# Kernel tuning notes

Hardware: AMD Instinct MI355X
Metric: run time of the kernel (lower is better)

Reference implementation:

```python
import jax, jax.numpy as jnp
import numpy as np

D_MODEL = 1024
N_HEADS = 16
D_K = D_MODEL // N_HEADS


def setup_inputs() -> dict:
    key = jax.random.key(0)
    k1, k2, k3 = jax.random.split(key, 3)
    x = jax.random.normal(k1, (4, 2048, D_MODEL), dtype=jnp.float32)
    # torch nn.Linear(d, 3d, bias=False): y = x @ W.T ; we store W.T directly as (in, out)
    w_qkv = jax.random.normal(k2, (D_MODEL, 3 * D_MODEL), dtype=jnp.float32) * (1.0 / np.sqrt(D_MODEL))
    w_out = jax.random.normal(k3, (D_MODEL, D_MODEL), dtype=jnp.float32) * (1.0 / np.sqrt(D_MODEL))
    return {"x": x, "w_qkv": w_qkv, "w_out": w_out}


def reference(x, w_qkv, w_out):
    B, T, D = x.shape
    qkv = jnp.einsum('btd,de->bte', x, w_qkv)  # (B,T,3D)
    q, k, v = jnp.split(qkv, 3, axis=-1)
    # split heads -> (B,H,T,d_k)
    def split_heads(t):
        return t.reshape(B, T, N_HEADS, D_K).transpose(0, 2, 1, 3)
    q, k, v = split_heads(q), split_heads(k), split_heads(v)
    scale = 1.0 / np.sqrt(D_K).astype(np.float32)
    scores = jnp.einsum('bhqd,bhkd->bhqk', q, k) * scale  # (B,H,T,T)
    causal = jnp.triu(jnp.full((T, T), -jnp.inf, dtype=scores.dtype), k=1)
    scores = scores + causal[None, None]
    weights = jax.nn.softmax(scores, axis=-1)
    attn = jnp.einsum('bhqk,bhkd->bhqd', weights, v)
    attn = attn.transpose(0, 2, 1, 3).reshape(B, T, D)
    return jnp.einsum('btd,de->bte', attn, w_out)
```

## Files before the change

### kernel.cpp

```cpp
#include <hip/hip_runtime.h>
#include <hip/hip_bf16.h>

typedef short short8 __attribute__((ext_vector_type(8)));
typedef float f32x4 __attribute__((ext_vector_type(4)));
typedef float f32x16 __attribute__((ext_vector_type(16)));

#define MFMA16(a, b, c) __builtin_amdgcn_mfma_f32_16x16x32_bf16((a), (b), (c), 0, 0, 0)
#define MFMA32(a, b, c) __builtin_amdgcn_mfma_f32_32x32x16_bf16((a), (b), (c), 0, 0, 0)

#define GLOAD16(gp, lp)                                                    \
    __builtin_amdgcn_global_load_lds(                                      \
        (const __attribute__((address_space(1))) unsigned int*)(gp),       \
        (__attribute__((address_space(3))) unsigned int*)(lp), 16, 0, 0)

__device__ __forceinline__ unsigned short f2b(float x) {
    unsigned int u = __float_as_uint(x);
    unsigned int r = u + 0x7FFFu + ((u >> 16) & 1u);
    return (unsigned short)(r >> 16);
}

#if __has_builtin(__builtin_amdgcn_cvt_pk_bf16_f32)
__device__ __forceinline__ unsigned pack2(float a, float b) {
    auto v = __builtin_amdgcn_cvt_pk_bf16_f32(a, b);
    unsigned u;
    __builtin_memcpy(&u, &v, 4);
    return u;
}
#else
__device__ __forceinline__ unsigned pack2(float a, float b) {
    return (unsigned)f2b(a) | ((unsigned)f2b(b) << 16);
}
#endif

__global__ __launch_bounds__(256) void cast4_kernel(const float* __restrict__ in,
                                                    unsigned short* __restrict__ out,
                                                    int n4) {
    int i = blockIdx.x * 256 + threadIdx.x;
    if (i < n4) {
        float4 v = ((const float4*)in)[i];
        ushort4 o;
        o.x = f2b(v.x); o.y = f2b(v.y); o.z = f2b(v.z); o.w = f2b(v.w);
        ((ushort4*)out)[i] = o;
    }
}

__global__ __launch_bounds__(256) void transpose_cast_f32(const float* __restrict__ in,
                                                          unsigned short* __restrict__ out,
                                                          int K, int N) {
    __shared__ unsigned short Ls[64 * 66];
    const int k0 = blockIdx.y * 64, n0 = blockIdx.x * 64;
    const int tid = threadIdx.x;
    const int krow = tid >> 4, nc4 = (tid & 15) * 4;
#pragma unroll
    for (int p = 0; p < 4; p++) {
        float4 v = *(const float4*)(in + (size_t)(k0 + krow + p * 16) * N + n0 + nc4);
        unsigned* d32 = (unsigned*)(Ls + (krow + p * 16) * 66 + nc4);
        d32[0] = pack2(v.x, v.y);
        d32[1] = pack2(v.z, v.w);
    }
    __syncthreads();
    const int n = tid >> 3, kc = (tid & 7) * 8;
#pragma unroll
    for (int p = 0; p < 2; p++) {
        int nn = n + p * 32;
        unsigned short w[8];
#pragma unroll
        for (int j = 0; j < 8; j++) w[j] = Ls[(kc + j) * 66 + nn];
        *(short8*)(out + (size_t)(n0 + nn) * K + k0 + kc) = *(short8*)w;
    }
}

__global__ __launch_bounds__(512, 2) void gemm_qkv(const unsigned short* __restrict__ A,
                                                   const unsigned short* __restrict__ Bt,
                                                   unsigned short* __restrict__ Qb,
                                                   unsigned short* __restrict__ Kb,
                                                   unsigned short* __restrict__ Vt) {
    __shared__ __align__(16) unsigned short smem[65536];

    const int tid  = threadIdx.x;
    const int wave = tid >> 6;
    const int lane = tid & 63;
    const int l32  = lane & 31;
    const int hi   = lane >> 5;
    const int wr   = wave >> 2;
    const int wc   = wave & 3;

    const int bid = blockIdx.x;
    const int sid = (bid & 7) * 48 + (bid >> 3);
    const int bx  = sid % 12;
    const int by  = sid / 12;
    const int m0 = by * 256;
    const int n0 = bx * 256;

    const int srow = tid >> 3;
    const int cswz = (((tid & 7) ^ ((tid >> 3) & 7)) * 8);
    const unsigned short* gA = A  + (size_t)(m0 + srow) * 1024 + cswz;
    const unsigned short* gB = Bt + (size_t)(n0 + srow) * 1024 + cswz;

#define STAGE_A(buf, h, kt) do {                                              \
        const unsigned short* _g = gA + (size_t)((h) * 128) * 1024 + (kt) * 64; \
        unsigned short* _l = smem + (buf) * 16384 + (h) * 8192 + wave * 512;  \
        GLOAD16(_g, _l);                                                      \
        GLOAD16(_g + 65536, _l + 4096);                                       \
    } while (0)
#define STAGE_B(buf, h, kt) do {                                              \
        const unsigned short* _g = gB + (size_t)((h) * 128) * 1024 + (kt) * 64; \
        unsigned short* _l = smem + 32768 + (buf) * 16384 + (h) * 8192 + wave * 512; \
        GLOAD16(_g, _l);                                                      \
        GLOAD16(_g + 65536, _l + 4096);                                       \
    } while (0)

    const int sw7  = l32 & 7;
    const int aoff = (wr * 128 + l32) * 64;
    const int boff = (wc * 64 + l32) * 64;

    f32x16 acc[4][2] = {};

    STAGE_A(0, 0, 0); STAGE_A(0, 1, 0); STAGE_B(0, 0, 0); STAGE_B(0, 1, 0);
    STAGE_B(1, 0, 1); STAGE_B(1, 1, 1); STAGE_A(1, 0, 1);
    asm volatile("s_waitcnt vmcnt(6)" ::: "memory");
    __builtin_amdgcn_s_barrier();

#pragma unroll
    for (int t = 0; t < 16; ++t) {
        const int b = t & 1;
        const unsigned short* Ab = smem + b * 16384;
        const unsigned short* Bb = smem + 32768 + b * 16384;

        short8 afLo[2][4], afHi[2][4], bf0[4], bf1[4];

#pragma unroll
        for (int rf = 0; rf < 2; ++rf)
#pragma unroll
            for (int ks = 0; ks < 4; ++ks)
                afLo[rf][ks] = *(const short8*)(Ab + aoff + rf * 2048 + (((ks * 2 + hi) ^ sw7) * 8));
#pragma unroll
        for (int ks = 0; ks < 4; ++ks)
            bf0[ks] = *(const short8*)(Bb + boff + (((ks * 2 + hi) ^ sw7) * 8));
        if (t + 1 < 16) STAGE_A(b ^ 1, 1, t + 1);
        __builtin_amdgcn_s_barrier();
        asm volatile("s_waitcnt lgkmcnt(0)" ::: "memory");
        __builtin_amdgcn_s_setprio(1);
#pragma unroll
        for (int ks = 0; ks < 4; ++ks) {
            acc[0][0] = MFMA32(afLo[0][ks], bf0[ks], acc[0][0]);
            acc[1][0] = MFMA32(afLo[1][ks], bf0[ks], acc[1][0]);
        }
        __builtin_amdgcn_s_setprio(0);
        __builtin_amdgcn_s_barrier();

#pragma unroll
        for (int ks = 0; ks < 4; ++ks)
            bf1[ks] = *(const short8*)(Bb + boff + 2048 + (((ks * 2 + hi) ^ sw7) * 8));
        __builtin_amdgcn_s_barrier();
        asm volatile("s_waitcnt lgkmcnt(0)" ::: "memory");
        __builtin_amdgcn_s_setprio(1);
#pragma unroll
        for (int ks = 0; ks < 4; ++ks) {
            acc[0][1] = MFMA32(afLo[0][ks], bf1[ks], acc[0][1]);
            acc[1][1] = MFMA32(afLo[1][ks], bf1[ks], acc[1][1]);
        }
        __builtin_amdgcn_s_setprio(0);
        __builtin_amdgcn_s_barrier();

#pragma unroll
        for (int rf = 0; rf < 2; ++rf)
#pragma unroll
            for (int ks = 0; ks < 4; ++ks)
                afHi[rf][ks] = *(const short8*)(Ab + aoff + (2 + rf) * 2048 + (((ks * 2 + hi) ^ sw7) * 8));
        if (t + 2 < 16) { STAGE_B(b, 0, t + 2); STAGE_B(b, 1, t + 2); }
        __builtin_amdgcn_s_barrier();
        asm volatile("s_waitcnt lgkmcnt(0)" ::: "memory");
        __builtin_amdgcn_s_setprio(1);
#pragma unroll
        for (int ks = 0; ks < 4; ++ks) {
            acc[2][0] = MFMA32(afHi[0][ks], bf0[ks], acc[2][0]);
            acc[3][0] = MFMA32(afHi[1][ks], bf0[ks], acc[3][0]);
        }
        __builtin_amdgcn_s_setprio(0);
        __builtin_amdgcn_s_barrier();

        if (t + 2 < 16) {
            STAGE_A(b, 0, t + 2);
            asm volatile("s_waitcnt vmcnt(6)" ::: "memory");
        } else {
            asm volatile("s_waitcnt vmcnt(0)" ::: "memory");
        }
        __builtin_amdgcn_s_barrier();
        __builtin_amdgcn_s_setprio(1);
#pragma unroll
        for (int ks = 0; ks < 4; ++ks) {
            acc[2][1] = MFMA32(afHi[0][ks], bf1[ks], acc[2][1]);
            acc[3][1] = MFMA32(afHi[1][ks], bf1[ks], acc[3][1]);
        }
        __builtin_amdgcn_s_setprio(0);
        __builtin_amdgcn_s_barrier();
    }
#undef STAGE_A
#undef STAGE_B

    if (n0 < 2048) {
        unsigned short* outp = (n0 < 1024) ? Qb : Kb;
        const int cb = (n0 < 1024) ? n0 : n0 - 1024;
        const float QS = (n0 < 1024) ? 0.125f * 1.44269504f : 1.0f;
#pragma unroll
        for (int rf = 0; rf < 4; ++rf)
#pragma unroll
            for (int cf = 0; cf < 2; ++cf)
#pragma unroll
                for (int r = 0; r < 16; ++r) {
                    int row = m0 + wr * 128 + rf * 32 + (r & 3) + 8 * (r >> 2) + 4 * hi;
                    int col = cb + wc * 64 + cf * 32 + l32;
                    outp[(size_t)row * 1024 + col] = f2b(acc[rf][cf][r] * QS);
                }
    } else {
        const int bb = m0 >> 11, t0b = m0 & 2047;
        const int hbase = (n0 - 2048) >> 6;
        unsigned short* reg = smem + wc * 16384;
#pragma unroll
        for (int rf = 0; rf < 4; ++rf)
#pragma unroll
            for (int cf = 0; cf < 2; ++cf)
#pragma unroll
                for (int rg = 0; rg < 4; ++rg) {
                    const int tl = wr * 128 + rf * 32 + rg * 8 + 4 * hi;
                    const int d  = cf * 32 + l32;
                    const int w  = d * 128 + ((tl >> 1) ^ (4 * (d & 7)));
                    uint2 v;
                    v.x = pack2(acc[rf][cf][4 * rg + 0], acc[rf][cf][4 * rg + 1]);
                    v.y = pack2(acc[rf][cf][4 * rg + 2], acc[rf][cf][4 * rg + 3]);
                    *(uint2*)(reg + 2 * w) = v;
                }
        __syncthreads();
#pragma unroll
        for (int it = 0; it < 16; ++it) {
            const int id = it * 512 + tid;
            const int hh = id >> 11, d = (id >> 5) & 63, k = id & 31;
            const int kb = k >> 2, kl = k & 3;
            const int xx = 4 * (d & 7);
            const unsigned short* bp = smem + hh * 16384 + 2 * (d * 128);
            uint2 lo  = *(const uint2*)(bp + 2 * ((16 * kb + 2 * kl) ^ xx));
            uint2 hi2 = *(const uint2*)(bp + 2 * ((16 * kb + 2 * kl + 8) ^ xx));
            uint2 parts[2] = {lo, hi2};
            short8 v; __builtin_memcpy(&v, parts, 16);
            *(short8*)(Vt + ((size_t)((bb * 16 + hbase + hh) * 64 + d)) * 2048 + t0b + k * 8) = v;
        }
    }
}

__global__ __launch_bounds__(512, 2) void gemm_out(const unsigned short* __restrict__ A,
                                                   const unsigned short* __restrict__ Bt,
                                                   float* __restrict__ C) {
    __shared__ __align__(16) unsigned short smem[49152];

    const int tid  = threadIdx.x;
    const int wave = tid >> 6;
    const int lane = tid & 63;
    const int l32  = lane & 31;
    const int hi   = lane >> 5;
    const int wr   = wave >> 2;
    const int wc   = wave & 3;

    const int bid = blockIdx.x;
    const int sid = (bid & 7) * 32 + (bid >> 3);
    const int bx  = sid & 3;
    const int by  = sid >> 2;
    const int m0 = by * 128;
    const int n0 = bx * 256;

    const int srow = tid >> 3;
    const int cswz = (((tid & 7) ^ ((tid >> 3) & 7)) * 8);
    const unsigned short* gA = A  + (size_t)(m0 + srow) * 1024 + cswz;
    const unsigned short* gB = Bt + (size_t)(n0 + srow) * 1024 + cswz;

#define STAGE_A(buf, h, kt) do {                                              \
        const unsigned short* _g = gA + (size_t)((h) * 64) * 1024 + (kt) * 64; \
        unsigned short* _l = smem + (buf) * 8192 + (h) * 4096 + wave * 512;   \
        GLOAD16(_g, _l);                                                      \
    } while (0)
#define STAGE_B(buf, h, kt) do {                                              \
        const unsigned short* _g = gB + (size_t)((h) * 128) * 1024 + (kt) * 64; \
        unsigned short* _l = smem + 16384 + (buf) * 16384 + (h) * 8192 + wave * 512; \
        GLOAD16(_g, _l);                                                      \
        GLOAD16(_g + 65536, _l + 4096);                                       \
    } while (0)

    const int sw7  = l32 & 7;
    const int aoff = (wr * 64 + l32) * 64;
    const int boff = (wc * 64 + l32) * 64;

    f32x16 acc[2][2] = {};

    STAGE_A(0, 0, 0); STAGE_A(0, 1, 0); STAGE_B(0, 0, 0); STAGE_B(0, 1, 0);
    STAGE_B(1, 0, 1); STAGE_B(1, 1, 1); STAGE_A(1, 0, 1);
    asm volatile("s_waitcnt vmcnt(5)" ::: "memory");
    __builtin_amdgcn_s_barrier();

#pragma unroll
    for (int t = 0; t < 16; ++t) {
        const int b = t & 1;
        const unsigned short* Ab = smem + b * 8192;
        const unsigned short* Bb = smem + 16384 + b * 16384;

        short8 af0[4], af1[4], bf0[4], bf1[4];

#pragma unroll
        for (int ks = 0; ks < 4; ++ks)
            af0[ks] = *(const short8*)(Ab + aoff + (((ks * 2 + hi) ^ sw7) * 8));
#pragma unroll
        for (int ks = 0; ks < 4; ++ks)
            bf0[ks] = *(const short8*)(Bb + boff + (((ks * 2 + hi) ^ sw7) * 8));
        if (t + 1 < 16) STAGE_A(b ^ 1, 1, t + 1);
        __builtin_amdgcn_s_barrier();
        asm volatile("s_waitcnt lgkmcnt(0)" ::: "memory");
        __builtin_amdgcn_s_setprio(1);
#pragma unroll
        for (int ks = 0; ks < 4; ++ks)
            acc[0][0] = MFMA32(af0[ks], bf0[ks], acc[0][0]);
        __builtin_amdgcn_s_setprio(0);
        __builtin_amdgcn_s_barrier();

#pragma unroll
        for (int ks = 0; ks < 4; ++ks)
            bf1[ks] = *(const short8*)(Bb + boff + 2048 + (((ks * 2 + hi) ^ sw7) * 8));
        __builtin_amdgcn_s_barrier();
        asm volatile("s_waitcnt lgkmcnt(0)" ::: "memory");
        __builtin_amdgcn_s_setprio(1);
#pragma unroll
        for (int ks = 0; ks < 4; ++ks)
            acc[0][1] = MFMA32(af0[ks], bf1[ks], acc[0][1]);
        __builtin_amdgcn_s_setprio(0);
        __builtin_amdgcn_s_barrier();

#pragma unroll
        for (int ks = 0; ks < 4; ++ks)
            af1[ks] = *(const short8*)(Ab + aoff + 2048 + (((ks * 2 + hi) ^ sw7) * 8));
        if (t + 2 < 16) { STAGE_B(b, 0, t + 2); STAGE_B(b, 1, t + 2); }
        __builtin_amdgcn_s_barrier();
        asm volatile("s_waitcnt lgkmcnt(0)" ::: "memory");
        __builtin_amdgcn_s_setprio(1);
#pragma unroll
        for (int ks = 0; ks < 4; ++ks)
            acc[1][0] = MFMA32(af1[ks], bf0[ks], acc[1][0]);
        __builtin_amdgcn_s_setprio(0);
        __builtin_amdgcn_s_barrier();

        if (t + 2 < 16) {
            STAGE_A(b, 0, t + 2);
            asm volatile("s_waitcnt vmcnt(5)" ::: "memory");
        } else {
            asm volatile("s_waitcnt vmcnt(0)" ::: "memory");
        }
        __builtin_amdgcn_s_barrier();
        __builtin_amdgcn_s_setprio(1);
#pragma unroll
        for (int ks = 0; ks < 4; ++ks)
            acc[1][1] = MFMA32(af1[ks], bf1[ks], acc[1][1]);
        __builtin_amdgcn_s_setprio(0);
        __builtin_amdgcn_s_barrier();
    }
#undef STAGE_A
#undef STAGE_B

#pragma unroll
    for (int rf = 0; rf < 2; ++rf)
#pragma unroll
        for (int cf = 0; cf < 2; ++cf)
#pragma unroll
            for (int r = 0; r < 16; ++r) {
                int row = m0 + wr * 64 + rf * 32 + (r & 3) + 8 * (r >> 2) + 4 * hi;
                int col = n0 + wc * 64 + cf * 32 + l32;
                C[(size_t)row * 1024 + col] = acc[rf][cf][r];
            }
}

__global__ __launch_bounds__(512, 8) void attention_kernel(const unsigned short* Qb,
                                                           const unsigned short* Kb,
                                                           const unsigned short* Vt,
                                                           unsigned short* attn) {
    const int T = 2048;
    const int bi = blockIdx.x;
    const int qb = 15 - (bi >> 6);
    const int hb = bi & 63;
    const int b = hb >> 4, h = hb & 15;
    const int tid = threadIdx.x, wave = tid >> 6, lane = tid & 63;
    const int l16 = lane & 15, quad = lane >> 4;
    const int qw0 = qb * 128 + wave * 16;

    const unsigned short* Qp  = Qb + (size_t)b * T * 1024 + h * 64;
    const unsigned short* Kp  = Kb + (size_t)b * T * 1024 + h * 64;
    const unsigned short* Vbh = Vt + ((size_t)(b * 16 + h) * 64) * 2048;

    __shared__ __align__(16) unsigned short smem[2][8192];

    short8 qf[2];
#pragma unroll
    for (int kd = 0; kd < 2; kd++)
        qf[kd] = *(const short8*)(Qp + (size_t)(qw0 + l16) * 1024 + kd * 32 + quad * 8);
    asm volatile("" ::: "memory");

    f32x4 o[4] = {};
    f32x4 o_l = {};
    const f32x4 fz = {};

    short8 onesf;
#pragma unroll
    for (int e = 0; e < 8; e++) onesf[e] = (short)0x3F80;

    const int srow = lane >> 2;
    const int scol = (((lane & 3) ^ ((lane >> 3) & 3)) * 8);
    const int sw8  = ((l16 >> 1) & 3) * 8;

    const unsigned short* gs;
    size_t ktstep, jstep;
    int lofs;
    if (wave < 4) {
        const int p = wave >> 1, cp = wave & 1;
        gs = Kp + (size_t)(cp * 32 + srow) * 1024 + p * 32 + scol;
        ktstep = (size_t)64 * 1024; jstep = (size_t)16 * 1024;
        lofs = p * 2048 + cp * 1024;
    } else {
        const int u = wave - 4, th = u >> 1, cp = u & 1;
        gs = Vbh + (size_t)(cp * 32 + srow) * 2048 + th * 32 + scol;
        ktstep = (size_t)64; jstep = (size_t)16 * 2048;
        lofs = 4096 + th * 2048 + cp * 1024;
    }

#define STAGE(bb, kt) do {                                   \
        const unsigned short* _g = gs + (size_t)(kt) * ktstep; \
        unsigned short* _l = &smem[bb][0] + lofs;             \
        GLOAD16(_g, _l);                                      \
        GLOAD16(_g + jstep, _l + 512);                        \
    } while (0)

    STAGE(0, 0);
    const int last = 2 * qb + 1;
    for (int kt = 0; kt <= last; kt++) {
        const int bsel = kt & 1;
        const int tk0 = kt * 64;
        if (kt < last) {
            STAGE(bsel ^ 1, kt + 1);
            asm volatile("s_waitcnt vmcnt(2)" ::: "memory");
        } else {
            asm volatile("s_waitcnt vmcnt(0)" ::: "memory");
        }
        __builtin_amdgcn_s_barrier();
        asm volatile("" ::: "memory");

        const unsigned short* Kb0 = &smem[bsel][0];
        const unsigned short* Kb1 = Kb0 + 2048;
        const unsigned short* Vb0 = Kb0 + 4096;

#pragma unroll
        for (int th = 0; th < 2; th++) {
            const int t0a = tk0 + th * 32;
            if (t0a > qw0 + 15) continue;
            const int t1 = t0a + 16;
            const bool act1 = (t1 <= qw0 + 15);

            f32x4 s0, s1;
            {
                const int row = (th * 2) * 16 + l16;
                short8 kf0 = *(const short8*)(Kb0 + row * 32 + (quad * 8 ^ sw8));
                short8 kf1 = *(const short8*)(Kb1 + row * 32 + (quad * 8 ^ sw8));
                s0 = MFMA16(kf0, qf[0], fz);
                s0 = MFMA16(kf1, qf[1], s0);
            }
            if (act1) {
                const int row = (th * 2 + 1) * 16 + l16;
                short8 kf0 = *(const short8*)(Kb0 + row * 32 + (quad * 8 ^ sw8));
                short8 kf1 = *(const short8*)(Kb1 + row * 32 + (quad * 8 ^ sw8));
                s1 = MFMA16(kf0, qf[0], fz);
                s1 = MFMA16(kf1, qf[1], s1);
            }

            unsigned u00, u01, u10, u11;
            {
                const bool full = (t0a + 15) <= qw0;
                float p[4];
#pragma unroll
                for (int r = 0; r < 4; r++) {
                    float e = __builtin_amdgcn_exp2f(s0[r]);
                    if (!full)
                        e = (t0a + quad * 4 + r <= qw0 + l16) ? e : 0.f;
                    p[r] = e;
                }
                u00 = pack2(p[0], p[1]);
                u01 = pack2(p[2], p[3]);
            }
            if (act1) {
                const bool full = (t1 + 15) <= qw0;
                float p[4];
#pragma unroll
                for (int r = 0; r < 4; r++) {
                    float e = __builtin_amdgcn_exp2f(s1[r]);
                    if (!full)
                        e = (t1 + quad * 4 + r <= qw0 + l16) ? e : 0.f;
                    p[r] = e;
                }
                u10 = pack2(p[0], p[1]);
                u11 = pack2(p[2], p[3]);
            } else {
                u10 = 0; u11 = 0;
            }

            unsigned pb[4] = {u00, u01, u10, u11};
            short8 pf; __builtin_memcpy(&pf, pb, 16);

            __builtin_amdgcn_s_setprio(1);
            o_l = MFMA16(onesf, pf, o_l);
#pragma unroll
            for (int dt = 0; dt < 4; dt++) {
                short8 vf = *(const short8*)(Vb0 + th * 2048 + (dt * 16 + l16) * 32 + (quad * 8 ^ sw8));
                o[dt] = MFMA16(vf, pf, o[dt]);
            }
            __builtin_amdgcn_s_setprio(0);
        }
        asm volatile("" ::: "memory");
        __builtin_amdgcn_s_barrier();
    }
#undef STAGE

    const float rl = 1.f / o_l[0];
    const int q = qw0 + l16;
#pragma unroll
    for (int dt = 0; dt < 4; dt++) {
        ushort4 wv;
        wv.x = f2b(o[dt][0] * rl);
        wv.y = f2b(o[dt][1] * rl);
        wv.z = f2b(o[dt][2] * rl);
        wv.w = f2b(o[dt][3] * rl);
        *(ushort4*)(attn + (size_t)(b * T + q) * 1024 + h * 64 + dt * 16 + quad * 4) = wv;
    }
}

extern "C" void kernel_launch(void* const* d_in, const int* in_sizes, int n_in,
                              void* d_out, int out_size, void* d_ws, size_t ws_size,
                              hipStream_t stream) {
    const float* x     = (const float*)d_in[0];
    const float* w_qkv = (const float*)d_in[1];
    const float* w_out = (const float*)d_in[2];
    float* out = (float*)d_out;

    const int M = 8192, D = 1024, E = 3072;
    const size_t MB = 1048576;

    char* ws = (char*)d_ws;
    unsigned short* xb    = (unsigned short*)ws;
    unsigned short* wqkvT = (unsigned short*)(ws + 16 * MB);
    unsigned short* woutT = (unsigned short*)(ws + 22 * MB);
    unsigned short* Qb    = (unsigned short*)(ws + 24 * MB);
    unsigned short* Kb    = (unsigned short*)(ws + 40 * MB);
    unsigned short* Vt    = (unsigned short*)(ws + 56 * MB);

    cast4_kernel<<<M * D / 4 / 256, 256, 0, stream>>>(x, xb, M * D / 4);
    transpose_cast_f32<<<dim3(E / 64, D / 64), 256, 0, stream>>>(w_qkv, wqkvT, D, E);
    transpose_cast_f32<<<dim3(D / 64, D / 64), 256, 0, stream>>>(w_out, woutT, D, D);

    gemm_qkv<<<dim3(384), 512, 0, stream>>>(xb, wqkvT, Qb, Kb, Vt);

    attention_kernel<<<dim3(1024), 512, 0, stream>>>(Qb, Kb, Vt, Qb);

    gemm_out<<<dim3(256), 512, 0, stream>>>(Qb, woutT, out);
}
```

Before: 248.3 us.

## Split QKV projection into separate QK and V GEMM kernels

Splits the fused QKV GEMM into two launches. gemm_qk handles the Q/K columns with 256 blocks of 256x256 tiles. It swaps the MFMA operands so each lane holds consecutive columns, which allows packed 8-byte bf16 stores instead of scalar 2-byte stores. gemm_v uses 128x256 tiles over 256 blocks for the V columns and keeps the LDS-staged transposed write into Vt. The intent is to balance work against the CU count (384 blocks does not map evenly onto the device) and to speed up the Q/K epilogue, at the cost of an extra kernel launch and reduced reuse in the smaller V tiles.

Result: no change. 245.5 us (-1.2%).

```diff
diff --git a/kernel.cpp b/kernel.cpp
--- a/kernel.cpp
+++ b/kernel.cpp
@@ -70,11 +70,10 @@
     }
 }
 
-__global__ __launch_bounds__(512, 2) void gemm_qkv(const unsigned short* __restrict__ A,
-                                                   const unsigned short* __restrict__ Bt,
-                                                   unsigned short* __restrict__ Qb,
-                                                   unsigned short* __restrict__ Kb,
-                                                   unsigned short* __restrict__ Vt) {
+__global__ __launch_bounds__(512, 2) void gemm_qk(const unsigned short* __restrict__ A,
+                                                  const unsigned short* __restrict__ Bt,
+                                                  unsigned short* __restrict__ Qb,
+                                                  unsigned short* __restrict__ Kb) {
     __shared__ __align__(16) unsigned short smem[65536];
 
     const int tid  = threadIdx.x;
@@ -86,9 +85,9 @@
     const int wc   = wave & 3;
 
     const int bid = blockIdx.x;
-    const int sid = (bid & 7) * 48 + (bid >> 3);
-    const int bx  = sid % 12;
-    const int by  = sid / 12;
+    const int sid = (bid & 7) * 32 + (bid >> 3);
+    const int bx  = sid & 7;
+    const int by  = sid >> 3;
     const int m0 = by * 256;
     const int n0 = bx * 256;
 
@@ -143,8 +142,8 @@
         __builtin_amdgcn_s_setprio(1);
 #pragma unroll
         for (int ks = 0; ks < 4; ++ks) {
-            acc[0][0] = MFMA32(afLo[0][ks], bf0[ks], acc[0][0]);
-            acc[1][0] = MFMA32(afLo[1][ks], bf0[ks], acc[1][0]);
+            acc[0][0] = MFMA32(bf0[ks], afLo[0][ks], acc[0][0]);
+            acc[1][0] = MFMA32(bf0[ks], afLo[1][ks], acc[1][0]);
         }
         __builtin_amdgcn_s_setprio(0);
         __builtin_amdgcn_s_barrier();
@@ -157,8 +156,8 @@
         __builtin_amdgcn_s_setprio(1);
 #pragma unroll
         for (int ks = 0; ks < 4; ++ks) {
-            acc[0][1] = MFMA32(afLo[0][ks], bf1[ks], acc[0][1]);
-            acc[1][1] = MFMA32(afLo[1][ks], bf1[ks], acc[1][1]);
+            acc[0][1] = MFMA32(bf1[ks], afLo[0][ks], acc[0][1]);
+            acc[1][1] = MFMA32(bf1[ks], afLo[1][ks], acc[1][1]);
         }
         __builtin_amdgcn_s_setprio(0);
         __builtin_amdgcn_s_barrier();
@@ -174,8 +173,8 @@
         __builtin_amdgcn_s_setprio(1);
 #pragma unroll
         for (int ks = 0; ks < 4; ++ks) {
-            acc[2][0] = MFMA32(afHi[0][ks], bf0[ks], acc[2][0]);
-            acc[3][0] = MFMA32(afHi[1][ks], bf0[ks], acc[3][0]);
+            acc[2][0] = MFMA32(bf0[ks], afHi[0][ks], acc[2][0]);
+            acc[3][0] = MFMA32(bf0[ks], afHi[1][ks], acc[3][0]);
         }
         __builtin_amdgcn_s_setprio(0);
         __builtin_amdgcn_s_barrier();
@@ -190,8 +189,8 @@
         __builtin_amdgcn_s_setprio(1);
 #pragma unroll
         for (int ks = 0; ks < 4; ++ks) {
-            acc[2][1] = MFMA32(afHi[0][ks], bf1[ks], acc[2][1]);
-            acc[3][1] = MFMA32(afHi[1][ks], bf1[ks], acc[3][1]);
+            acc[2][1] = MFMA32(bf1[ks], afHi[0][ks], acc[2][1]);
+            acc[3][1] = MFMA32(bf1[ks], afHi[1][ks], acc[3][1]);
         }
         __builtin_amdgcn_s_setprio(0);
         __builtin_amdgcn_s_barrier();
@@ -199,52 +198,169 @@
 #undef STAGE_A
 #undef STAGE_B
 
-    if (n0 < 2048) {
-        unsigned short* outp = (n0 < 1024) ? Qb : Kb;
-        const int cb = (n0 < 1024) ? n0 : n0 - 1024;
-        const float QS = (n0 < 1024) ? 0.125f * 1.44269504f : 1.0f;
-#pragma unroll
-        for (int rf = 0; rf < 4; ++rf)
-#pragma unroll
-            for (int cf = 0; cf < 2; ++cf)
-#pragma unroll
-                for (int r = 0; r < 16; ++r) {
-                    int row = m0 + wr * 128 + rf * 32 + (r & 3) + 8 * (r >> 2) + 4 * hi;
-                    int col = cb + wc * 64 + cf * 32 + l32;
-                    outp[(size_t)row * 1024 + col] = f2b(acc[rf][cf][r] * QS);
-                }
-    } else {
-        const int bb = m0 >> 11, t0b = m0 & 2047;
-        const int hbase = (n0 - 2048) >> 6;
-        unsigned short* reg = smem + wc * 16384;
-#pragma unroll
-        for (int rf = 0; rf < 4; ++rf)
-#pragma unroll
-            for (int cf = 0; cf < 2; ++cf)
-#pragma unroll
-                for (int rg = 0; rg < 4; ++rg) {
-                    const int tl = wr * 128 + rf * 32 + rg * 8 + 4 * hi;
-                    const int d  = cf * 32 + l32;
-                    const int w  = d * 128 + ((tl >> 1) ^ (4 * (d & 7)));
-                    uint2 v;
-                    v.x = pack2(acc[rf][cf][4 * rg + 0], acc[rf][cf][4 * rg + 1]);
-                    v.y = pack2(acc[rf][cf][4 * rg + 2], acc[rf][cf][4 * rg + 3]);
-                    *(uint2*)(reg + 2 * w) = v;
-                }
-        __syncthreads();
-#pragma unroll
-        for (int it = 0; it < 16; ++it) {
-            const int id = it * 512 + tid;
-            const int hh = id >> 11, d = (id >> 5) & 63, k = id & 31;
-            const int kb = k >> 2, kl = k & 3;
-            const int xx = 4 * (d & 7);
-            const unsigned short* bp = smem + hh * 16384 + 2 * (d * 128);
-            uint2 lo  = *(const uint2*)(bp + 2 * ((16 * kb + 2 * kl) ^ xx));
-            uint2 hi2 = *(const uint2*)(bp + 2 * ((16 * kb + 2 * kl + 8) ^ xx));
-            uint2 parts[2] = {lo, hi2};
-            short8 v; __builtin_memcpy(&v, parts, 16);
-            *(short8*)(Vt + ((size_t)((bb * 16 + hbase + hh) * 64 + d)) * 2048 + t0b + k * 8) = v;
-        }
+    unsigned short* outp = (n0 < 1024) ? Qb : Kb;
+    const int cb = (n0 < 1024) ? n0 : n0 - 1024;
+    const float QS = (n0 < 1024) ? 0.125f * 1.44269504f : 1.0f;
+#pragma unroll
+    for (int rf = 0; rf < 4; ++rf) {
+        const int row = m0 + wr * 128 + rf * 32 + l32;
+#pragma unroll
+        for (int cf = 0; cf < 2; ++cf)
+#pragma unroll
+            for (int g = 0; g < 4; ++g) {
+                const int col = cb + wc * 64 + cf * 32 + g * 8 + 4 * hi;
+                uint2 v;
+                v.x = pack2(acc[rf][cf][4 * g + 0] * QS, acc[rf][cf][4 * g + 1] * QS);
+                v.y = pack2(acc[rf][cf][4 * g + 2] * QS, acc[rf][cf][4 * g + 3] * QS);
+                *(uint2*)(outp + (size_t)row * 1024 + col) = v;
+            }
+    }
+}
+
+__global__ __launch_bounds__(512, 2) void gemm_v(const unsigned short* __restrict__ A,
+                                                 const unsigned short* __restrict__ Bt,
+                                                 unsigned short* __restrict__ Vt) {
+    __shared__ __align__(16) unsigned short smem[49152];
+
+    const int tid  = threadIdx.x;
+    const int wave = tid >> 6;
+    const int lane = tid & 63;
+    const int l32  = lane & 31;
+    const int hi   = lane >> 5;
+    const int wr   = wave >> 2;
+    const int wc   = wave & 3;
+
+    const int bid = blockIdx.x;
+    const int sid = (bid & 7) * 32 + (bid >> 3);
+    const int bx  = sid & 3;
+    const int by  = sid >> 2;
+    const int m0 = by * 128;
+    const int n0 = bx * 256;
+
+    const int srow = tid >> 3;
+    const int cswz = (((tid & 7) ^ ((tid >> 3) & 7)) * 8);
+    const unsigned short* gA = A  + (size_t)(m0 + srow) * 1024 + cswz;
+    const unsigned short* gB = Bt + (size_t)(n0 + srow) * 1024 + cswz;
+
+#define STAGE_A(buf, h, kt) do {                                              \
+        const unsigned short* _g = gA + (size_t)((h) * 64) * 1024 + (kt) * 64; \
+        unsigned short* _l = smem + (buf) * 8192 + (h) * 4096 + wave * 512;   \
+        GLOAD16(_g, _l);                                                      \
+    } while (0)
+#define STAGE_B(buf, h, kt) do {                                              \
+        const unsigned short* _g = gB + (size_t)((h) * 128) * 1024 + (kt) * 64; \
+        unsigned short* _l = smem + 16384 + (buf) * 16384 + (h) * 8192 + wave * 512; \
+        GLOAD16(_g, _l);                                                      \
+        GLOAD16(_g + 65536, _l + 4096);                                       \
+    } while (0)
+
+    const int sw7  = l32 & 7;
+    const int aoff = (wr * 64 + l32) * 64;
+    const int boff = (wc * 64 + l32) * 64;
+
+    f32x16 acc[2][2] = {};
+
+    STAGE_A(0, 0, 0); STAGE_A(0, 1, 0); STAGE_B(0, 0, 0); STAGE_B(0, 1, 0);
+    STAGE_B(1, 0, 1); STAGE_B(1, 1, 1); STAGE_A(1, 0, 1);
+    asm volatile("s_waitcnt vmcnt(5)" ::: "memory");
+    __builtin_amdgcn_s_barrier();
+
+#pragma unroll
+    for (int t = 0; t < 16; ++t) {
+        const int b = t & 1;
+        const unsigned short* Ab = smem + b * 8192;
+        const unsigned short* Bb = smem + 16384 + b * 16384;
+
+        short8 af0[4], af1[4], bf0[4], bf1[4];
+
+#pragma unroll
+        for (int ks = 0; ks < 4; ++ks)
+            af0[ks] = *(const short8*)(Ab + aoff + (((ks * 2 + hi) ^ sw7) * 8));
+#pragma unroll
+        for (int ks = 0; ks < 4; ++ks)
+            bf0[ks] = *(const short8*)(Bb + boff + (((ks * 2 + hi) ^ sw7) * 8));
+        if (t + 1 < 16) STAGE_A(b ^ 1, 1, t + 1);
+        __builtin_amdgcn_s_barrier();
+        asm volatile("s_waitcnt lgkmcnt(0)" ::: "memory");
+        __builtin_amdgcn_s_setprio(1);
+#pragma unroll
+        for (int ks = 0; ks < 4; ++ks)
+            acc[0][0] = MFMA32(af0[ks], bf0[ks], acc[0][0]);
+        __builtin_amdgcn_s_setprio(0);
+        __builtin_amdgcn_s_barrier();
+
+#pragma unroll
+        for (int ks = 0; ks < 4; ++ks)
+            bf1[ks] = *(const short8*)(Bb + boff + 2048 + (((ks * 2 + hi) ^ sw7) * 8));
+        __builtin_amdgcn_s_barrier();
+        asm volatile("s_waitcnt lgkmcnt(0)" ::: "memory");
+        __builtin_amdgcn_s_setprio(1);
+#pragma unroll
+        for (int ks = 0; ks < 4; ++ks)
+            acc[0][1] = MFMA32(af0[ks], bf1[ks], acc[0][1]);
+        __builtin_amdgcn_s_setprio(0);
+        __builtin_amdgcn_s_barrier();
+
+#pragma unroll
+        for (int ks = 0; ks < 4; ++ks)
+            af1[ks] = *(const short8*)(Ab + aoff + 2048 + (((ks * 2 + hi) ^ sw7) * 8));
+        if (t + 2 < 16) { STAGE_B(b, 0, t + 2); STAGE_B(b, 1, t + 2); }
+        __builtin_amdgcn_s_barrier();
+        asm volatile("s_waitcnt lgkmcnt(0)" ::: "memory");
+        __builtin_amdgcn_s_setprio(1);
+#pragma unroll
+        for (int ks = 0; ks < 4; ++ks)
+            acc[1][0] = MFMA32(af1[ks], bf0[ks], acc[1][0]);
+        __builtin_amdgcn_s_setprio(0);
+        __builtin_amdgcn_s_barrier();
+
+        if (t + 2 < 16) {
+            STAGE_A(b, 0, t + 2);
+            asm volatile("s_waitcnt vmcnt(5)" ::: "memory");
+        } else {
+            asm volatile("s_waitcnt vmcnt(0)" ::: "memory");
+        }
+        __builtin_amdgcn_s_barrier();
+        __builtin_amdgcn_s_setprio(1);
+#pragma unroll
+        for (int ks = 0; ks < 4; ++ks)
+            acc[1][1] = MFMA32(af1[ks], bf1[ks], acc[1][1]);
+        __builtin_amdgcn_s_setprio(0);
+        __builtin_amdgcn_s_barrier();
+    }
+#undef STAGE_A
+#undef STAGE_B
+
+    const int bb = m0 >> 11, t0b = m0 & 2047;
+    const int hbase = n0 >> 6;
+    unsigned short* reg = smem + wc * 8192;
+#pragma unroll
+    for (int rf = 0; rf < 2; ++rf)
+#pragma unroll
+        for (int cf = 0; cf < 2; ++cf)
+#pragma unroll
+            for (int rg = 0; rg < 4; ++rg) {
+                const int tl = wr * 64 + rf * 32 + rg * 8 + 4 * hi;
+                const int d  = cf * 32 + l32;
+                const int w  = d * 64 + ((tl >> 1) ^ (4 * (d & 7)));
+                uint2 v;
+                v.x = pack2(acc[rf][cf][4 * rg + 0], acc[rf][cf][4 * rg + 1]);
+                v.y = pack2(acc[rf][cf][4 * rg + 2], acc[rf][cf][4 * rg + 3]);
+                *(uint2*)(reg + 2 * w) = v;
+            }
+    __syncthreads();
+#pragma unroll
+    for (int it = 0; it < 8; ++it) {
+        const int id = it * 512 + tid;
+        const int hh = id >> 10, d = (id >> 4) & 63, k = id & 15;
+        const int kb = k >> 2, kl = k & 3;
+        const int xx = 4 * (d & 7);
+        const unsigned short* bp = smem + hh * 8192 + 2 * (d * 64);
+        uint2 lo  = *(const uint2*)(bp + 2 * ((16 * kb + 2 * kl) ^ xx));
+        uint2 hi2 = *(const uint2*)(bp + 2 * ((16 * kb + 2 * kl + 8) ^ xx));
+        uint2 parts[2] = {lo, hi2};
+        short8 v; __builtin_memcpy(&v, parts, 16);
+        *(short8*)(Vt + ((size_t)((bb * 16 + hbase + hh) * 64 + d)) * 2048 + t0b + k * 8) = v;
     }
 }
 
@@ -557,7 +673,8 @@
     transpose_cast_f32<<<dim3(E / 64, D / 64), 256, 0, stream>>>(w_qkv, wqkvT, D, E);
     transpose_cast_f32<<<dim3(D / 64, D / 64), 256, 0, stream>>>(w_out, woutT, D, D);
 
-    gemm_qkv<<<dim3(384), 512, 0, stream>>>(xb, wqkvT, Qb, Kb, Vt);
+    gemm_qk<<<dim3(256), 512, 0, stream>>>(xb, wqkvT, Qb, Kb);
+    gemm_v<<<dim3(256), 512, 0, stream>>>(xb, wqkvT + (size_t)2048 * 1024, Vt);
 
     attention_kernel<<<dim3(1024), 512, 0, stream>>>(Qb, Kb, Vt, Qb);
 
```
